# Kernel optimization log

Hardware: AMD Instinct MI355X
Metric: run time of the kernel (lower is better)

## Reference

```python
import jax, jax.numpy as jnp
import numpy as np
import math

# SH band constants (match torch source)
A0C0 = math.pi * (1.0 / math.sqrt(4.0 * math.pi))
A1C1 = (2.0 * math.pi / math.sqrt(3.0)) * (math.sqrt(3.0) / math.sqrt(4.0 * math.pi))
A2C2 = (2.0 * math.pi / math.sqrt(8.0)) * (3.0 * math.sqrt(5.0) / math.sqrt(12.0 * math.pi))
AMBIENT = 0.8
SIGMA = 1e-4   # BlendParams defaults
GAMMA = 1e-4
BG = (1.0, 1.0, 1.0)
ZNEAR, ZFAR = 1.0, 100.0
EPS = 1e-10

V, F = 100000, 200000
N, H, W, K = 2, 512, 512, 8


def setup_inputs() -> dict:
    key = jax.random.key(0)
    ks = jax.random.split(key, 8)
    verts_normals = jax.random.normal(ks[0], (V, 3), dtype=jnp.float32)
    verts_colors = jax.random.uniform(ks[1], (V, 3), dtype=jnp.float32)
    sh_coeffs = jax.random.normal(ks[2], (1, 9, 3), dtype=jnp.float32) * 0.3
    bary = jax.random.uniform(ks[3], (N, H, W, K, 3), dtype=jnp.float32) + 1e-3
    bary_coords = bary / jnp.sum(bary, axis=-1, keepdims=True)  # convex weights
    zbuf = ZNEAR + (ZFAR - ZNEAR) * jax.random.uniform(ks[4], (N, H, W, K), dtype=jnp.float32)
    dists = jax.random.normal(ks[5], (N, H, W, K), dtype=jnp.float32) * 1e-4  # signed pixel-to-edge dists
    faces = jax.random.randint(ks[6], (F, 3), 0, V, dtype=jnp.int64 if jax.config.jax_enable_x64 else jnp.int32)
    pix_to_face = jax.random.randint(ks[7], (N, H, W, K), -20000, F,
                                     dtype=jnp.int64 if jax.config.jax_enable_x64 else jnp.int32)
    return {"verts_normals": verts_normals, "verts_colors": verts_colors,
            "sh_coeffs": sh_coeffs, "bary_coords": bary_coords,
            "zbuf": zbuf, "dists": dists, "faces": faces, "pix_to_face": pix_to_face}


def _forward(verts_normals, verts_colors, sh_coeffs, bary_coords, zbuf, dists,
             faces, pix_to_face):
    # --- per-vertex SH shading ---
    sh = sh_coeffs.at[..., 0, :].add(AMBIENT)          # (1,9,3), ambient term
    nrm = jnp.maximum(jnp.linalg.norm(verts_normals, axis=-1, keepdims=True), 1e-6)
    n = verts_normals / nrm                            # (V,3)
    nx, ny, nz = n[..., 0], n[..., 1], n[..., 2]
    Y = jnp.stack([
        jnp.full(nx.shape, A0C0, dtype=n.dtype),
        -A1C1 * ny,
        A1C1 * nz,
        -A1C1 * nx,
        A2C2 * nx * ny,
        -A2C2 * ny * nz,
        A2C2 * 0.5 / math.sqrt(3.0) * (3.0 * nz * nz - 1.0),
        -A2C2 * nx * nz,
        A2C2 * 0.5 * (nx * nx - ny * ny),
    ], axis=-1)                                        # (V,9)
    shading = jnp.einsum('vn,nc->vc', Y, sh[0])        # (V,3)
    verts_colors_shaded = verts_colors * shading       # (V,3)

    # --- face gather + barycentric interpolation ---
    face_colors = verts_colors_shaded[faces]           # (F,3,3)
    mask = pix_to_face >= 0                            # (N,H,W,K)
    idx = jnp.where(mask, pix_to_face, 0)
    pix_face_vals = face_colors[idx]                   # (N,H,W,K,3,3)
    colors = jnp.sum(bary_coords[..., None] * pix_face_vals, axis=-2)  # (N,H,W,K,3)
    colors = jnp.where(mask[..., None], colors, 0.0)

    # --- softmax RGB blend ---
    maskf = mask.astype(colors.dtype)
    prob = jax.nn.sigmoid(-dists / SIGMA) * maskf                       # (N,H,W,K)
    alpha = jnp.prod(1.0 - prob, axis=-1)                               # (N,H,W)
    z_inv = (ZFAR - zbuf) / (ZFAR - ZNEAR) * maskf
    z_inv_max = jnp.maximum(jnp.max(z_inv, axis=-1, keepdims=True), EPS)
    weights_num = prob * jnp.exp((z_inv - z_inv_max) / GAMMA)
    delta = jnp.exp((EPS - z_inv_max) / GAMMA)                          # background weight
    denom = jnp.sum(weights_num, axis=-1, keepdims=True) + delta
    weighted_colors = jnp.sum(weights_num[..., None] * colors, axis=-2)  # (N,H,W,3)
    bg = jnp.asarray(BG, dtype=colors.dtype)
    rgb = (weighted_colors + delta * bg) / denom
    return jnp.concatenate([rgb, (1.0 - alpha)[..., None]], axis=-1)    # (N,H,W,4)


def reference(verts_normals, verts_colors, sh_coeffs, bary_coords, zbuf, dists,
              faces, pix_to_face):
    return _forward(verts_normals, verts_colors, sh_coeffs, bary_coords, zbuf,
                    dists, faces, pix_to_face)
```

## Files before the change

kernel.cpp:

```cpp
#include <hip/hip_runtime.h>
#include <math.h>

typedef float    f4  __attribute__((ext_vector_type(4)));
typedef int      i4  __attribute__((ext_vector_type(4)));
typedef _Float16 hf4 __attribute__((ext_vector_type(4)));

namespace {

constexpr float kA0C0     = 0.8862269254527580f;
constexpr float kA1C1     = 1.7724538509055159f;
constexpr float kA2C2     = 2.4270324670f;
constexpr float kAmbient  = 0.8f;
constexpr float kInvSigma = 1e4f;
constexpr float kInvGamma = 1e4f;
constexpr float kEps      = 1e-10f;
constexpr float kZfar     = 100.0f;
constexpr float kInvZrng  = 1.0f / 99.0f;

__global__ void shade_face_kernel(const float* __restrict__ vn,
                                  const float* __restrict__ vc,
                                  const float* __restrict__ sh,
                                  const int* __restrict__ faces,
                                  hf4* __restrict__ fc, int F) {
  int f = blockIdx.x * blockDim.x + threadIdx.x;
  if (f >= F) return;
  float s0r = sh[0] + kAmbient, s0g = sh[1] + kAmbient, s0b = sh[2] + kAmbient;
  int vid[3] = {faces[3 * f + 0], faces[3 * f + 1], faces[3 * f + 2]};
#pragma unroll
  for (int j = 0; j < 3; ++j) {
    int v = vid[j];
    float nx = vn[3 * v + 0], ny = vn[3 * v + 1], nz = vn[3 * v + 2];
    float nrm = fmaxf(sqrtf(nx * nx + ny * ny + nz * nz), 1e-6f);
    nx /= nrm; ny /= nrm; nz /= nrm;
    float Y1 = -kA1C1 * ny, Y2 = kA1C1 * nz, Y3 = -kA1C1 * nx;
    float Y4 =  kA2C2 * nx * ny, Y5 = -kA2C2 * ny * nz;
    float Y6 =  kA2C2 * (0.5f / 1.7320508075688772f) * (3.0f * nz * nz - 1.0f);
    float Y7 = -kA2C2 * nx * nz, Y8 = kA2C2 * 0.5f * (nx * nx - ny * ny);
    float r = kA0C0 * s0r + Y1 * sh[3] + Y2 * sh[6]  + Y3 * sh[9]  + Y4 * sh[12]
            + Y5 * sh[15] + Y6 * sh[18] + Y7 * sh[21] + Y8 * sh[24];
    float g = kA0C0 * s0g + Y1 * sh[4] + Y2 * sh[7]  + Y3 * sh[10] + Y4 * sh[13]
            + Y5 * sh[16] + Y6 * sh[19] + Y7 * sh[22] + Y8 * sh[25];
    float b = kA0C0 * s0b + Y1 * sh[5] + Y2 * sh[8]  + Y3 * sh[11] + Y4 * sh[14]
            + Y5 * sh[17] + Y6 * sh[20] + Y7 * sh[23] + Y8 * sh[26];
    hf4 o;
    o.x = (_Float16)(vc[3 * v + 0] * r);
    o.y = (_Float16)(vc[3 * v + 1] * g);
    o.z = (_Float16)(vc[3 * v + 2] * b);
    o.w = (_Float16)0.0f;
    fc[3 * f + j] = o;
  }
}

__global__ void __launch_bounds__(256) blend_kernel(
    const float* __restrict__ bary,
    const f4* __restrict__ zb4,
    const f4* __restrict__ ds4,
    const i4* __restrict__ pf4,
    const hf4* __restrict__ fc,
    f4* __restrict__ out, int P) {
  int p = blockIdx.x * blockDim.x + threadIdx.x;
  if (p >= P) return;

  i4 fA = __builtin_nontemporal_load(pf4 + 2 * p);
  i4 fB = __builtin_nontemporal_load(pf4 + 2 * p + 1);
  f4 zA = __builtin_nontemporal_load(zb4 + 2 * p);
  f4 zB = __builtin_nontemporal_load(zb4 + 2 * p + 1);
  f4 dA = __builtin_nontemporal_load(ds4 + 2 * p);
  f4 dB = __builtin_nontemporal_load(ds4 + 2 * p + 1);
  int   fk[8] = {fA.x, fA.y, fA.z, fA.w, fB.x, fB.y, fB.z, fB.w};
  float z[8]  = {zA.x, zA.y, zA.z, zA.w, zB.x, zB.y, zB.z, zB.w};
  float d[8]  = {dA.x, dA.y, dA.z, dA.w, dB.x, dB.y, dB.z, dB.w};

  float pr[8], zi[8];
  float maxz = kEps, alpha = 1.0f;
#pragma unroll
  for (int k = 0; k < 8; ++k) {
    bool m = fk[k] >= 0;
    float e = __expf(d[k] * kInvSigma);
    float prv = m ? 1.0f / (1.0f + e) : 0.0f;
    pr[k] = prv;
    alpha *= 1.0f - prv;
    float zv = m ? (kZfar - z[k]) * kInvZrng : 0.0f;
    zi[k] = zv;
    maxz = fmaxf(maxz, zv);
  }

  float delta = __expf((kEps - maxz) * kInvGamma);
  float denom = delta;
  float cr = 0.0f, cg = 0.0f, cb = 0.0f;
#pragma unroll
  for (int k = 0; k < 8; ++k) {
    float w = pr[k] * __expf((zi[k] - maxz) * kInvGamma);
    denom += w;
    if (w != 0.0f) {
      int t = 8 * p + k;
      float b0 = bary[3 * t + 0], b1 = bary[3 * t + 1], b2 = bary[3 * t + 2];
      hf4 v0 = fc[3 * fk[k] + 0];
      hf4 v1 = fc[3 * fk[k] + 1];
      hf4 v2 = fc[3 * fk[k] + 2];
      cr += w * (b0 * (float)v0.x + b1 * (float)v1.x + b2 * (float)v2.x);
      cg += w * (b0 * (float)v0.y + b1 * (float)v1.y + b2 * (float)v2.y);
      cb += w * (b0 * (float)v0.z + b1 * (float)v1.z + b2 * (float)v2.z);
    }
  }

  f4 o;
  o.x = (cr + delta) / denom;
  o.y = (cg + delta) / denom;
  o.z = (cb + delta) / denom;
  o.w = 1.0f - alpha;
  __builtin_nontemporal_store(o, out + p);
}

}

extern "C" void kernel_launch(void* const* d_in, const int* in_sizes, int n_in,
                              void* d_out, int out_size, void* d_ws, size_t ws_size,
                              hipStream_t stream) {
  const float* vn    = (const float*)d_in[0];
  const float* vc    = (const float*)d_in[1];
  const float* sh    = (const float*)d_in[2];
  const float* bary  = (const float*)d_in[3];
  const float* zbuf  = (const float*)d_in[4];
  const float* dists = (const float*)d_in[5];
  const int*   faces = (const int*)d_in[6];
  const int*   p2f   = (const int*)d_in[7];

  const int F = in_sizes[6] / 3;
  const int P = in_sizes[4] / 8;

  hf4* fc = (hf4*)d_ws;

  shade_face_kernel<<<(F + 255) / 256, 256, 0, stream>>>(vn, vc, sh, faces, fc, F);
  blend_kernel<<<(P + 255) / 256, 256, 0, stream>>>(
      bary, (const f4*)zbuf, (const f4*)dists, (const i4*)p2f, fc, (f4*)d_out, P);
}
```

Baseline: 149.9 us.

## Process two pixels per thread and gather only the top-two weighted faces

The blend kernel now handles two pixels per thread, half the grid apart. For each pixel it picks the two largest non-zero softmax weights and issues their bary and face-color gathers unconditionally, with no data-dependent branching. A slow path recomputes everything and gathers all faces when more than two weights are non-zero. Weights whose exponent falls below -88 are treated as zero, and reciprocals use rcp intrinsics. The aim is fewer divergent scattered gathers and more memory-level parallelism, at the cost of higher register pressure, duplicated work on the slow path, and an odd P leaving the last pixel unprocessed.

```diff
diff --git a/kernel.cpp b/kernel.cpp
--- a/kernel.cpp
+++ b/kernel.cpp
@@ -16,6 +16,7 @@
 constexpr float kEps      = 1e-10f;
 constexpr float kZfar     = 100.0f;
 constexpr float kInvZrng  = 1.0f / 99.0f;
+constexpr float kExpCut   = -88.0f;
 
 __global__ void shade_face_kernel(const float* __restrict__ vn,
                                   const float* __restrict__ vc,
@@ -51,47 +52,76 @@
   }
 }
 
-__global__ void __launch_bounds__(256) blend_kernel(
-    const float* __restrict__ bary,
-    const f4* __restrict__ zb4,
-    const f4* __restrict__ ds4,
-    const i4* __restrict__ pf4,
-    const hf4* __restrict__ fc,
-    f4* __restrict__ out, int P) {
-  int p = blockIdx.x * blockDim.x + threadIdx.x;
-  if (p >= P) return;
-
-  i4 fA = __builtin_nontemporal_load(pf4 + 2 * p);
-  i4 fB = __builtin_nontemporal_load(pf4 + 2 * p + 1);
-  f4 zA = __builtin_nontemporal_load(zb4 + 2 * p);
-  f4 zB = __builtin_nontemporal_load(zb4 + 2 * p + 1);
-  f4 dA = __builtin_nontemporal_load(ds4 + 2 * p);
-  f4 dB = __builtin_nontemporal_load(ds4 + 2 * p + 1);
-  int   fk[8] = {fA.x, fA.y, fA.z, fA.w, fB.x, fB.y, fB.z, fB.w};
-  float z[8]  = {zA.x, zA.y, zA.z, zA.w, zB.x, zB.y, zB.z, zB.w};
-  float d[8]  = {dA.x, dA.y, dA.z, dA.w, dB.x, dB.y, dB.z, dB.w};
-
+struct Sel {
+  float w1, w2, delta, denom, alpha, maxz;
+  int t1, f1, t2, f2, cnt;
+};
+
+__device__ __forceinline__ Sel phase1(int p, i4 fa, i4 fb, f4 za, f4 zb,
+                                      f4 da, f4 db) {
+  int   fk[8] = {fa.x, fa.y, fa.z, fa.w, fb.x, fb.y, fb.z, fb.w};
+  float zz[8] = {za.x, za.y, za.z, za.w, zb.x, zb.y, zb.z, zb.w};
+  float dd[8] = {da.x, da.y, da.z, da.w, db.x, db.y, db.z, db.w};
   float pr[8], zi[8];
   float maxz = kEps, alpha = 1.0f;
 #pragma unroll
   for (int k = 0; k < 8; ++k) {
     bool m = fk[k] >= 0;
-    float e = __expf(d[k] * kInvSigma);
-    float prv = m ? 1.0f / (1.0f + e) : 0.0f;
+    float e = __expf(dd[k] * kInvSigma);
+    float prv = m ? __builtin_amdgcn_rcpf(1.0f + e) : 0.0f;
     pr[k] = prv;
     alpha *= 1.0f - prv;
-    float zv = m ? (kZfar - z[k]) * kInvZrng : 0.0f;
+    float zv = m ? (kZfar - zz[k]) * kInvZrng : 0.0f;
     zi[k] = zv;
     maxz = fmaxf(maxz, zv);
   }
-
-  float delta = __expf((kEps - maxz) * kInvGamma);
-  float denom = delta;
-  float cr = 0.0f, cg = 0.0f, cb = 0.0f;
+  Sel s;
+  s.maxz  = maxz;
+  s.alpha = alpha;
+  s.delta = __expf((kEps - maxz) * kInvGamma);
+  float denom = s.delta;
+  float m1 = -1.0f, m2 = -1.0f;
+  int k1 = 0, k2 = 0, f1 = 0, f2 = 0, cnt = 0;
 #pragma unroll
   for (int k = 0; k < 8; ++k) {
-    float w = pr[k] * __expf((zi[k] - maxz) * kInvGamma);
+    float edz = (zi[k] - maxz) * kInvGamma;
+    float w = (edz > kExpCut) ? pr[k] * __expf(edz) : 0.0f;
     denom += w;
+    cnt += (w != 0.0f) ? 1 : 0;
+    bool g1 = w > m1, g2 = w > m2;
+    m2 = g1 ? m1 : (g2 ? w : m2);
+    k2 = g1 ? k1 : (g2 ? k : k2);
+    f2 = g1 ? f1 : (g2 ? fk[k] : f2);
+    m1 = g1 ? w : m1;
+    k1 = g1 ? k : k1;
+    f1 = g1 ? fk[k] : f1;
+  }
+  s.denom = denom;
+  s.w1 = fmaxf(m1, 0.0f);
+  s.w2 = fmaxf(m2, 0.0f);
+  s.t1 = 8 * p + k1;  s.f1 = max(f1, 0);
+  s.t2 = 8 * p + k2;  s.f2 = max(f2, 0);
+  s.cnt = cnt;
+  return s;
+}
+
+__device__ __forceinline__ void slowpath(int p, i4 fa, i4 fb, f4 za, f4 zb,
+                                         f4 da, f4 db, float maxz,
+                                         const float* __restrict__ bary,
+                                         const hf4* __restrict__ fc,
+                                         float& cr, float& cg, float& cb) {
+  int   fk[8] = {fa.x, fa.y, fa.z, fa.w, fb.x, fb.y, fb.z, fb.w};
+  float zz[8] = {za.x, za.y, za.z, za.w, zb.x, zb.y, zb.z, zb.w};
+  float dd[8] = {da.x, da.y, da.z, da.w, db.x, db.y, db.z, db.w};
+  cr = cg = cb = 0.0f;
+#pragma unroll
+  for (int k = 0; k < 8; ++k) {
+    bool m = fk[k] >= 0;
+    float e = __expf(dd[k] * kInvSigma);
+    float prv = m ? __builtin_amdgcn_rcpf(1.0f + e) : 0.0f;
+    float zv = m ? (kZfar - zz[k]) * kInvZrng : 0.0f;
+    float edz = (zv - maxz) * kInvGamma;
+    float w = (edz > kExpCut) ? prv * __expf(edz) : 0.0f;
     if (w != 0.0f) {
       int t = 8 * p + k;
       float b0 = bary[3 * t + 0], b1 = bary[3 * t + 1], b2 = bary[3 * t + 2];
@@ -103,13 +133,79 @@
       cb += w * (b0 * (float)v0.z + b1 * (float)v1.z + b2 * (float)v2.z);
     }
   }
-
-  f4 o;
-  o.x = (cr + delta) / denom;
-  o.y = (cg + delta) / denom;
-  o.z = (cb + delta) / denom;
-  o.w = 1.0f - alpha;
-  __builtin_nontemporal_store(o, out + p);
+}
+
+__global__ void __launch_bounds__(256, 4) blend_kernel(
+    const float* __restrict__ bary,
+    const f4* __restrict__ zb4,
+    const f4* __restrict__ ds4,
+    const i4* __restrict__ pf4,
+    const hf4* __restrict__ fc,
+    f4* __restrict__ out, int Phalf) {
+  int t = blockIdx.x * blockDim.x + threadIdx.x;
+  if (t >= Phalf) return;
+  int p0 = t, p1 = t + Phalf;
+
+  i4 fA0 = __builtin_nontemporal_load(pf4 + 2 * p0);
+  i4 fA1 = __builtin_nontemporal_load(pf4 + 2 * p0 + 1);
+  i4 fB0 = __builtin_nontemporal_load(pf4 + 2 * p1);
+  i4 fB1 = __builtin_nontemporal_load(pf4 + 2 * p1 + 1);
+  f4 zA0 = __builtin_nontemporal_load(zb4 + 2 * p0);
+  f4 zA1 = __builtin_nontemporal_load(zb4 + 2 * p0 + 1);
+  f4 zB0 = __builtin_nontemporal_load(zb4 + 2 * p1);
+  f4 zB1 = __builtin_nontemporal_load(zb4 + 2 * p1 + 1);
+  f4 dA0 = __builtin_nontemporal_load(ds4 + 2 * p0);
+  f4 dA1 = __builtin_nontemporal_load(ds4 + 2 * p0 + 1);
+  f4 dB0 = __builtin_nontemporal_load(ds4 + 2 * p1);
+  f4 dB1 = __builtin_nontemporal_load(ds4 + 2 * p1 + 1);
+
+  Sel sA = phase1(p0, fA0, fA1, zA0, zA1, dA0, dA1);
+  Sel sB = phase1(p1, fB0, fB1, zB0, zB1, dB0, dB1);
+
+  const float* bA1 = bary + 3 * sA.t1;
+  const float* bA2 = bary + 3 * sA.t2;
+  const float* bB1 = bary + 3 * sB.t1;
+  const float* bB2 = bary + 3 * sB.t2;
+  float a1b0 = bA1[0], a1b1 = bA1[1], a1b2 = bA1[2];
+  float a2b0 = bA2[0], a2b1 = bA2[1], a2b2 = bA2[2];
+  float b1b0 = bB1[0], b1b1 = bB1[1], b1b2 = bB1[2];
+  float b2b0 = bB2[0], b2b1 = bB2[1], b2b2 = bB2[2];
+  hf4 A1v0 = fc[3 * sA.f1 + 0], A1v1 = fc[3 * sA.f1 + 1], A1v2 = fc[3 * sA.f1 + 2];
+  hf4 A2v0 = fc[3 * sA.f2 + 0], A2v1 = fc[3 * sA.f2 + 1], A2v2 = fc[3 * sA.f2 + 2];
+  hf4 B1v0 = fc[3 * sB.f1 + 0], B1v1 = fc[3 * sB.f1 + 1], B1v2 = fc[3 * sB.f1 + 2];
+  hf4 B2v0 = fc[3 * sB.f2 + 0], B2v1 = fc[3 * sB.f2 + 1], B2v2 = fc[3 * sB.f2 + 2];
+
+  float crA = sA.w1 * (a1b0 * (float)A1v0.x + a1b1 * (float)A1v1.x + a1b2 * (float)A1v2.x)
+            + sA.w2 * (a2b0 * (float)A2v0.x + a2b1 * (float)A2v1.x + a2b2 * (float)A2v2.x);
+  float cgA = sA.w1 * (a1b0 * (float)A1v0.y + a1b1 * (float)A1v1.y + a1b2 * (float)A1v2.y)
+            + sA.w2 * (a2b0 * (float)A2v0.y + a2b1 * (float)A2v1.y + a2b2 * (float)A2v2.y);
+  float cbA = sA.w1 * (a1b0 * (float)A1v0.z + a1b1 * (float)A1v1.z + a1b2 * (float)A1v2.z)
+            + sA.w2 * (a2b0 * (float)A2v0.z + a2b1 * (float)A2v1.z + a2b2 * (float)A2v2.z);
+  float crB = sB.w1 * (b1b0 * (float)B1v0.x + b1b1 * (float)B1v1.x + b1b2 * (float)B1v2.x)
+            + sB.w2 * (b2b0 * (float)B2v0.x + b2b1 * (float)B2v1.x + b2b2 * (float)B2v2.x);
+  float cgB = sB.w1 * (b1b0 * (float)B1v0.y + b1b1 * (float)B1v1.y + b1b2 * (float)B1v2.y)
+            + sB.w2 * (b2b0 * (float)B2v0.y + b2b1 * (float)B2v1.y + b2b2 * (float)B2v2.y);
+  float cbB = sB.w1 * (b1b0 * (float)B1v0.z + b1b1 * (float)B1v1.z + b1b2 * (float)B1v2.z)
+            + sB.w2 * (b2b0 * (float)B2v0.z + b2b1 * (float)B2v1.z + b2b2 * (float)B2v2.z);
+
+  if (sA.cnt > 2)
+    slowpath(p0, fA0, fA1, zA0, zA1, dA0, dA1, sA.maxz, bary, fc, crA, cgA, cbA);
+  if (sB.cnt > 2)
+    slowpath(p1, fB0, fB1, zB0, zB1, dB0, dB1, sB.maxz, bary, fc, crB, cgB, cbB);
+
+  float rdA = __builtin_amdgcn_rcpf(sA.denom);
+  float rdB = __builtin_amdgcn_rcpf(sB.denom);
+  f4 oA, oB;
+  oA.x = (crA + sA.delta) * rdA;
+  oA.y = (cgA + sA.delta) * rdA;
+  oA.z = (cbA + sA.delta) * rdA;
+  oA.w = 1.0f - sA.alpha;
+  oB.x = (crB + sB.delta) * rdB;
+  oB.y = (cgB + sB.delta) * rdB;
+  oB.z = (cbB + sB.delta) * rdB;
+  oB.w = 1.0f - sB.alpha;
+  __builtin_nontemporal_store(oA, out + p0);
+  __builtin_nontemporal_store(oB, out + p1);
 }
 
 }
@@ -128,10 +224,11 @@
 
   const int F = in_sizes[6] / 3;
   const int P = in_sizes[4] / 8;
+  const int Phalf = P / 2;
 
   hf4* fc = (hf4*)d_ws;
 
   shade_face_kernel<<<(F + 255) / 256, 256, 0, stream>>>(vn, vc, sh, faces, fc, F);
-  blend_kernel<<<(P + 255) / 256, 256, 0, stream>>>(
-      bary, (const f4*)zbuf, (const f4*)dists, (const i4*)p2f, fc, (f4*)d_out, P);
-}
+  blend_kernel<<<(Phalf + 255) / 256, 256, 0, stream>>>(
+      bary, (const f4*)zbuf, (const f4*)dists, (const i4*)p2f, fc, (f4*)d_out, Phalf);
+}
```

Result: slower. 153.7 us (+2.6%).

## Split pixels across thread pairs and repack face color table into 16+4 bytes

Applied to the files above, without the earlier changes.

The blend kernel now gives each pixel's 8 layers to two threads of 4 layers each, combining the max, alpha product and color sums through lane shuffles. Each thread loads its barycentrics as three aligned float4 vectors instead of scalar loads. The per-face color table is repacked from three 8-byte half4 records into one 16-byte half8 record plus one float, so a face gather touches fewer bytes and transactions. It also skips exponentials below a cutoff and uses hardware reciprocals, which adds shuffle work, leaves half the lanes idle at the store, and slightly lowers precision.

```diff
diff --git a/kernel.cpp b/kernel.cpp
--- a/kernel.cpp
+++ b/kernel.cpp
@@ -3,7 +3,7 @@
 
 typedef float    f4  __attribute__((ext_vector_type(4)));
 typedef int      i4  __attribute__((ext_vector_type(4)));
-typedef _Float16 hf4 __attribute__((ext_vector_type(4)));
+typedef _Float16 hf8 __attribute__((ext_vector_type(8)));
 
 namespace {
 
@@ -16,16 +16,19 @@
 constexpr float kEps      = 1e-10f;
 constexpr float kZfar     = 100.0f;
 constexpr float kInvZrng  = 1.0f / 99.0f;
+constexpr float kExpCut   = -88.0f;
 
 __global__ void shade_face_kernel(const float* __restrict__ vn,
                                   const float* __restrict__ vc,
                                   const float* __restrict__ sh,
                                   const int* __restrict__ faces,
-                                  hf4* __restrict__ fc, int F) {
+                                  hf8* __restrict__ tabA,
+                                  float* __restrict__ tabB, int F) {
   int f = blockIdx.x * blockDim.x + threadIdx.x;
   if (f >= F) return;
   float s0r = sh[0] + kAmbient, s0g = sh[1] + kAmbient, s0b = sh[2] + kAmbient;
   int vid[3] = {faces[3 * f + 0], faces[3 * f + 1], faces[3 * f + 2]};
+  float col[9];
 #pragma unroll
   for (int j = 0; j < 3; ++j) {
     int v = vid[j];
@@ -42,74 +45,90 @@
             + Y5 * sh[16] + Y6 * sh[19] + Y7 * sh[22] + Y8 * sh[25];
     float b = kA0C0 * s0b + Y1 * sh[5] + Y2 * sh[8]  + Y3 * sh[11] + Y4 * sh[14]
             + Y5 * sh[17] + Y6 * sh[20] + Y7 * sh[23] + Y8 * sh[26];
-    hf4 o;
-    o.x = (_Float16)(vc[3 * v + 0] * r);
-    o.y = (_Float16)(vc[3 * v + 1] * g);
-    o.z = (_Float16)(vc[3 * v + 2] * b);
-    o.w = (_Float16)0.0f;
-    fc[3 * f + j] = o;
+    col[3 * j + 0] = vc[3 * v + 0] * r;
+    col[3 * j + 1] = vc[3 * v + 1] * g;
+    col[3 * j + 2] = vc[3 * v + 2] * b;
   }
+  hf8 a;
+#pragma unroll
+  for (int i = 0; i < 8; ++i) a[i] = (_Float16)col[i];
+  tabA[f] = a;
+  tabB[f] = col[8];
 }
 
-__global__ void __launch_bounds__(256) blend_kernel(
-    const float* __restrict__ bary,
-    const f4* __restrict__ zb4,
-    const f4* __restrict__ ds4,
-    const i4* __restrict__ pf4,
-    const hf4* __restrict__ fc,
-    f4* __restrict__ out, int P) {
-  int p = blockIdx.x * blockDim.x + threadIdx.x;
-  if (p >= P) return;
+__global__ void blend_kernel(const f4* __restrict__ bary4,
+                             const f4* __restrict__ zb4,
+                             const f4* __restrict__ ds4,
+                             const i4* __restrict__ pf4,
+                             const hf8* __restrict__ tabA,
+                             const float* __restrict__ tabB,
+                             f4* __restrict__ out, int T) {
+  int t = blockIdx.x * blockDim.x + threadIdx.x;
+  if (t >= T) return;
 
-  i4 fA = __builtin_nontemporal_load(pf4 + 2 * p);
-  i4 fB = __builtin_nontemporal_load(pf4 + 2 * p + 1);
-  f4 zA = __builtin_nontemporal_load(zb4 + 2 * p);
-  f4 zB = __builtin_nontemporal_load(zb4 + 2 * p + 1);
-  f4 dA = __builtin_nontemporal_load(ds4 + 2 * p);
-  f4 dB = __builtin_nontemporal_load(ds4 + 2 * p + 1);
-  int   fk[8] = {fA.x, fA.y, fA.z, fA.w, fB.x, fB.y, fB.z, fB.w};
-  float z[8]  = {zA.x, zA.y, zA.z, zA.w, zB.x, zB.y, zB.z, zB.w};
-  float d[8]  = {dA.x, dA.y, dA.z, dA.w, dB.x, dB.y, dB.z, dB.w};
+  i4 fv = __builtin_nontemporal_load(pf4 + t);
+  f4 zv = __builtin_nontemporal_load(zb4 + t);
+  f4 dv = __builtin_nontemporal_load(ds4 + t);
+  f4 b0 = __builtin_nontemporal_load(bary4 + 3 * t);
+  f4 b1 = __builtin_nontemporal_load(bary4 + 3 * t + 1);
+  f4 b2 = __builtin_nontemporal_load(bary4 + 3 * t + 2);
 
-  float pr[8], zi[8];
-  float maxz = kEps, alpha = 1.0f;
+  int   fk[4] = {fv.x, fv.y, fv.z, fv.w};
+  float zz[4] = {zv.x, zv.y, zv.z, zv.w};
+  float dd[4] = {dv.x, dv.y, dv.z, dv.w};
+  float bw[12] = {b0.x, b0.y, b0.z, b0.w, b1.x, b1.y, b1.z, b1.w,
+                  b2.x, b2.y, b2.z, b2.w};
+
+  float pr[4], zi[4];
+  float mx = 0.0f, om = 1.0f;
 #pragma unroll
-  for (int k = 0; k < 8; ++k) {
-    bool m = fk[k] >= 0;
-    float e = __expf(d[k] * kInvSigma);
-    float prv = m ? 1.0f / (1.0f + e) : 0.0f;
-    pr[k] = prv;
-    alpha *= 1.0f - prv;
-    float zv = m ? (kZfar - z[k]) * kInvZrng : 0.0f;
-    zi[k] = zv;
-    maxz = fmaxf(maxz, zv);
+  for (int j = 0; j < 4; ++j) {
+    bool m = fk[j] >= 0;
+    float e = __expf(dd[j] * kInvSigma);
+    float prv = m ? __builtin_amdgcn_rcpf(1.0f + e) : 0.0f;
+    pr[j] = prv;
+    om *= 1.0f - prv;
+    float zva = m ? (kZfar - zz[j]) * kInvZrng : 0.0f;
+    zi[j] = zva;
+    mx = fmaxf(mx, zva);
   }
 
-  float delta = __expf((kEps - maxz) * kInvGamma);
-  float denom = delta;
-  float cr = 0.0f, cg = 0.0f, cb = 0.0f;
+  float mxp = fmaxf(fmaxf(mx, __shfl_xor(mx, 1)), kEps);
+  float alpha_om = om * __shfl_xor(om, 1);
+
+  float delta = __expf((kEps - mxp) * kInvGamma);
+  float den = 0.0f, cr = 0.0f, cg = 0.0f, cb = 0.0f;
 #pragma unroll
-  for (int k = 0; k < 8; ++k) {
-    float w = pr[k] * __expf((zi[k] - maxz) * kInvGamma);
-    denom += w;
+  for (int j = 0; j < 4; ++j) {
+    float edz = (zi[j] - mxp) * kInvGamma;
+    float w = (edz > kExpCut) ? pr[j] * __expf(edz) : 0.0f;
+    den += w;
     if (w != 0.0f) {
-      int t = 8 * p + k;
-      float b0 = bary[3 * t + 0], b1 = bary[3 * t + 1], b2 = bary[3 * t + 2];
-      hf4 v0 = fc[3 * fk[k] + 0];
-      hf4 v1 = fc[3 * fk[k] + 1];
-      hf4 v2 = fc[3 * fk[k] + 2];
-      cr += w * (b0 * (float)v0.x + b1 * (float)v1.x + b2 * (float)v2.x);
-      cg += w * (b0 * (float)v0.y + b1 * (float)v1.y + b2 * (float)v2.y);
-      cb += w * (b0 * (float)v0.z + b1 * (float)v1.z + b2 * (float)v2.z);
+      int f = fk[j];
+      hf8  a  = tabA[f];
+      float vb = tabB[f];
+      float w0 = bw[3 * j + 0], w1 = bw[3 * j + 1], w2 = bw[3 * j + 2];
+      cr += w * (w0 * (float)a[0] + w1 * (float)a[3] + w2 * (float)a[6]);
+      cg += w * (w0 * (float)a[1] + w1 * (float)a[4] + w2 * (float)a[7]);
+      cb += w * (w0 * (float)a[2] + w1 * (float)a[5] + w2 * vb);
     }
   }
 
-  f4 o;
-  o.x = (cr + delta) / denom;
-  o.y = (cg + delta) / denom;
-  o.z = (cb + delta) / denom;
-  o.w = 1.0f - alpha;
-  __builtin_nontemporal_store(o, out + p);
+  den += __shfl_xor(den, 1);
+  cr  += __shfl_xor(cr, 1);
+  cg  += __shfl_xor(cg, 1);
+  cb  += __shfl_xor(cb, 1);
+
+  if ((t & 1) == 0) {
+    den += delta;
+    float inv = __builtin_amdgcn_rcpf(den);
+    f4 o;
+    o.x = (cr + delta) * inv;
+    o.y = (cg + delta) * inv;
+    o.z = (cb + delta) * inv;
+    o.w = 1.0f - alpha_om;
+    __builtin_nontemporal_store(o, out + (t >> 1));
+  }
 }
 
 }
@@ -127,11 +146,14 @@
   const int*   p2f   = (const int*)d_in[7];
 
   const int F = in_sizes[6] / 3;
-  const int P = in_sizes[4] / 8;
+  const int T = in_sizes[4] / 4;
 
-  hf4* fc = (hf4*)d_ws;
+  hf8*   tabA = (hf8*)d_ws;
+  float* tabB = (float*)((char*)d_ws + ((size_t)F * 16 + 255 & ~(size_t)255));
 
-  shade_face_kernel<<<(F + 255) / 256, 256, 0, stream>>>(vn, vc, sh, faces, fc, F);
-  blend_kernel<<<(P + 255) / 256, 256, 0, stream>>>(
-      bary, (const f4*)zbuf, (const f4*)dists, (const i4*)p2f, fc, (f4*)d_out, P);
+  shade_face_kernel<<<(F + 255) / 256, 256, 0, stream>>>(vn, vc, sh, faces,
+                                                         tabA, tabB, F);
+  blend_kernel<<<(T + 255) / 256, 256, 0, stream>>>(
+      (const f4*)bary, (const f4*)zbuf, (const f4*)dists, (const i4*)p2f,
+      tabA, tabB, (f4*)d_out, T);
 }
```

Result: slower. 154.2 us (+2.9%).

## Pack face colors into 16B+4B tables and software-pipeline a persistent blend loop

Applied to the files above, without the earlier changes.

The per-face color table changes from three 8-byte fp16 entries to one 16-byte fp16x8 entry plus a separate fp32 for the ninth channel, so each gather touches fewer cache lines. The blend kernel becomes a grid-stride persistent loop with 1024 blocks that prefetches the next pixel's inputs while processing the current one. It also skips the exp when its argument would underflow and uses hardware reciprocals instead of divides. The ninth color channel now uses a different precision from the rest, and the fixed grid size may underfill or overfill the GPU.

```diff
diff --git a/kernel.cpp b/kernel.cpp
--- a/kernel.cpp
+++ b/kernel.cpp
@@ -3,7 +3,7 @@
 
 typedef float    f4  __attribute__((ext_vector_type(4)));
 typedef int      i4  __attribute__((ext_vector_type(4)));
-typedef _Float16 hf4 __attribute__((ext_vector_type(4)));
+typedef _Float16 hf8 __attribute__((ext_vector_type(8)));
 
 namespace {
 
@@ -16,16 +16,20 @@
 constexpr float kEps      = 1e-10f;
 constexpr float kZfar     = 100.0f;
 constexpr float kInvZrng  = 1.0f / 99.0f;
+constexpr float kExpCut   = -88.0f;
+constexpr int   kBlendBlocks = 1024;
 
 __global__ void shade_face_kernel(const float* __restrict__ vn,
                                   const float* __restrict__ vc,
                                   const float* __restrict__ sh,
                                   const int* __restrict__ faces,
-                                  hf4* __restrict__ fc, int F) {
+                                  hf8* __restrict__ tabA,
+                                  float* __restrict__ tabB, int F) {
   int f = blockIdx.x * blockDim.x + threadIdx.x;
   if (f >= F) return;
   float s0r = sh[0] + kAmbient, s0g = sh[1] + kAmbient, s0b = sh[2] + kAmbient;
   int vid[3] = {faces[3 * f + 0], faces[3 * f + 1], faces[3 * f + 2]};
+  float col[9];
 #pragma unroll
   for (int j = 0; j < 3; ++j) {
     int v = vid[j];
@@ -42,45 +46,52 @@
             + Y5 * sh[16] + Y6 * sh[19] + Y7 * sh[22] + Y8 * sh[25];
     float b = kA0C0 * s0b + Y1 * sh[5] + Y2 * sh[8]  + Y3 * sh[11] + Y4 * sh[14]
             + Y5 * sh[17] + Y6 * sh[20] + Y7 * sh[23] + Y8 * sh[26];
-    hf4 o;
-    o.x = (_Float16)(vc[3 * v + 0] * r);
-    o.y = (_Float16)(vc[3 * v + 1] * g);
-    o.z = (_Float16)(vc[3 * v + 2] * b);
-    o.w = (_Float16)0.0f;
-    fc[3 * f + j] = o;
+    col[3 * j + 0] = vc[3 * v + 0] * r;
+    col[3 * j + 1] = vc[3 * v + 1] * g;
+    col[3 * j + 2] = vc[3 * v + 2] * b;
   }
+  hf8 a;
+#pragma unroll
+  for (int i = 0; i < 8; ++i) a[i] = (_Float16)col[i];
+  tabA[f] = a;
+  tabB[f] = col[8];
 }
 
-__global__ void __launch_bounds__(256) blend_kernel(
+struct Px { i4 f0, f1; f4 z0, z1, d0, d1; };
+
+__device__ __forceinline__ Px load_px(const i4* __restrict__ pf4,
+                                      const f4* __restrict__ zb4,
+                                      const f4* __restrict__ ds4, int p) {
+  Px s;
+  s.f0 = __builtin_nontemporal_load(pf4 + 2 * p);
+  s.f1 = __builtin_nontemporal_load(pf4 + 2 * p + 1);
+  s.z0 = __builtin_nontemporal_load(zb4 + 2 * p);
+  s.z1 = __builtin_nontemporal_load(zb4 + 2 * p + 1);
+  s.d0 = __builtin_nontemporal_load(ds4 + 2 * p);
+  s.d1 = __builtin_nontemporal_load(ds4 + 2 * p + 1);
+  return s;
+}
+
+__device__ __forceinline__ void process_px(
+    int p, const Px& s,
     const float* __restrict__ bary,
-    const f4* __restrict__ zb4,
-    const f4* __restrict__ ds4,
-    const i4* __restrict__ pf4,
-    const hf4* __restrict__ fc,
-    f4* __restrict__ out, int P) {
-  int p = blockIdx.x * blockDim.x + threadIdx.x;
-  if (p >= P) return;
-
-  i4 fA = __builtin_nontemporal_load(pf4 + 2 * p);
-  i4 fB = __builtin_nontemporal_load(pf4 + 2 * p + 1);
-  f4 zA = __builtin_nontemporal_load(zb4 + 2 * p);
-  f4 zB = __builtin_nontemporal_load(zb4 + 2 * p + 1);
-  f4 dA = __builtin_nontemporal_load(ds4 + 2 * p);
-  f4 dB = __builtin_nontemporal_load(ds4 + 2 * p + 1);
-  int   fk[8] = {fA.x, fA.y, fA.z, fA.w, fB.x, fB.y, fB.z, fB.w};
-  float z[8]  = {zA.x, zA.y, zA.z, zA.w, zB.x, zB.y, zB.z, zB.w};
-  float d[8]  = {dA.x, dA.y, dA.z, dA.w, dB.x, dB.y, dB.z, dB.w};
+    const hf8* __restrict__ tabA,
+    const float* __restrict__ tabB,
+    f4* __restrict__ out) {
+  int   fk[8] = {s.f0.x, s.f0.y, s.f0.z, s.f0.w, s.f1.x, s.f1.y, s.f1.z, s.f1.w};
+  float zz[8] = {s.z0.x, s.z0.y, s.z0.z, s.z0.w, s.z1.x, s.z1.y, s.z1.z, s.z1.w};
+  float dd[8] = {s.d0.x, s.d0.y, s.d0.z, s.d0.w, s.d1.x, s.d1.y, s.d1.z, s.d1.w};
 
   float pr[8], zi[8];
   float maxz = kEps, alpha = 1.0f;
 #pragma unroll
   for (int k = 0; k < 8; ++k) {
     bool m = fk[k] >= 0;
-    float e = __expf(d[k] * kInvSigma);
-    float prv = m ? 1.0f / (1.0f + e) : 0.0f;
+    float e = __expf(dd[k] * kInvSigma);
+    float prv = m ? __builtin_amdgcn_rcpf(1.0f + e) : 0.0f;
     pr[k] = prv;
     alpha *= 1.0f - prv;
-    float zv = m ? (kZfar - z[k]) * kInvZrng : 0.0f;
+    float zv = m ? (kZfar - zz[k]) * kInvZrng : 0.0f;
     zi[k] = zv;
     maxz = fmaxf(maxz, zv);
   }
@@ -90,26 +101,53 @@
   float cr = 0.0f, cg = 0.0f, cb = 0.0f;
 #pragma unroll
   for (int k = 0; k < 8; ++k) {
-    float w = pr[k] * __expf((zi[k] - maxz) * kInvGamma);
+    float edz = (zi[k] - maxz) * kInvGamma;
+    float w = (edz > kExpCut) ? pr[k] * __expf(edz) : 0.0f;
     denom += w;
     if (w != 0.0f) {
       int t = 8 * p + k;
       float b0 = bary[3 * t + 0], b1 = bary[3 * t + 1], b2 = bary[3 * t + 2];
-      hf4 v0 = fc[3 * fk[k] + 0];
-      hf4 v1 = fc[3 * fk[k] + 1];
-      hf4 v2 = fc[3 * fk[k] + 2];
-      cr += w * (b0 * (float)v0.x + b1 * (float)v1.x + b2 * (float)v2.x);
-      cg += w * (b0 * (float)v0.y + b1 * (float)v1.y + b2 * (float)v2.y);
-      cb += w * (b0 * (float)v0.z + b1 * (float)v1.z + b2 * (float)v2.z);
+      hf8  a  = tabA[fk[k]];
+      float vb = tabB[fk[k]];
+      cr += w * (b0 * (float)a[0] + b1 * (float)a[3] + b2 * (float)a[6]);
+      cg += w * (b0 * (float)a[1] + b1 * (float)a[4] + b2 * (float)a[7]);
+      cb += w * (b0 * (float)a[2] + b1 * (float)a[5] + b2 * vb);
     }
   }
 
+  float inv = __builtin_amdgcn_rcpf(denom);
   f4 o;
-  o.x = (cr + delta) / denom;
-  o.y = (cg + delta) / denom;
-  o.z = (cb + delta) / denom;
+  o.x = (cr + delta) * inv;
+  o.y = (cg + delta) * inv;
+  o.z = (cb + delta) * inv;
   o.w = 1.0f - alpha;
   __builtin_nontemporal_store(o, out + p);
+}
+
+__global__ void __launch_bounds__(256, 4) blend_kernel(
+    const float* __restrict__ bary,
+    const f4* __restrict__ zb4,
+    const f4* __restrict__ ds4,
+    const i4* __restrict__ pf4,
+    const hf8* __restrict__ tabA,
+    const float* __restrict__ tabB,
+    f4* __restrict__ out, int P) {
+  int tid = blockIdx.x * blockDim.x + threadIdx.x;
+  int stride = gridDim.x * blockDim.x;
+  if (tid >= P) return;
+
+  int p = tid;
+  Px cur = load_px(pf4, zb4, ds4, p);
+  while (true) {
+    int pn = p + stride;
+    bool more = pn < P;
+    Px nxt;
+    if (more) nxt = load_px(pf4, zb4, ds4, pn);
+    process_px(p, cur, bary, tabA, tabB, out);
+    if (!more) break;
+    p = pn;
+    cur = nxt;
+  }
 }
 
 }
@@ -129,9 +167,12 @@
   const int F = in_sizes[6] / 3;
   const int P = in_sizes[4] / 8;
 
-  hf4* fc = (hf4*)d_ws;
+  hf8*   tabA = (hf8*)d_ws;
+  float* tabB = (float*)((char*)d_ws + (((size_t)F * 16 + 255) & ~(size_t)255));
 
-  shade_face_kernel<<<(F + 255) / 256, 256, 0, stream>>>(vn, vc, sh, faces, fc, F);
-  blend_kernel<<<(P + 255) / 256, 256, 0, stream>>>(
-      bary, (const f4*)zbuf, (const f4*)dists, (const i4*)p2f, fc, (f4*)d_out, P);
+  shade_face_kernel<<<(F + 255) / 256, 256, 0, stream>>>(vn, vc, sh, faces,
+                                                         tabA, tabB, F);
+  blend_kernel<<<kBlendBlocks, 256, 0, stream>>>(
+      bary, (const f4*)zbuf, (const f4*)dists, (const i4*)p2f,
+      tabA, tabB, (f4*)d_out, P);
 }
```

Measured after the change: 153.0 us. +2.1%, slower.
